# Kernel optimization log

Measured on AMD Instinct MI355X. Metric: run time of the kernel, lower is better.

The kernel has to match this reference:

```python
import jax, jax.numpy as jnp
import numpy as np

N = 8192
W_MEAN, W_VAR = 0.15, 0.25
DELTA_THETA_S = 30.0
B_S = 0.5
R_I = 18.0
F_V = 0.12
DELTA_V = 12.0
THETA_INIT = 30.0
E_L0, C_M0, G0, TAU_G0 = -65.0, 1.0, 0.7, 2.0


def setup_inputs() -> dict:
    key = jax.random.key(0)
    k_x, k_v, k_g, k_w = jax.random.split(key, 4)
    x_in = jax.random.normal(k_x, (N,), dtype=jnp.float32)
    v = jax.random.normal(k_v, (N,), dtype=jnp.float32)
    g = jax.random.uniform(k_g, (N,), dtype=jnp.float32)
    theta_s = THETA_INIT * jnp.ones((N,), dtype=jnp.float32)
    w = W_MEAN - W_VAR + 2.0 * W_VAR * jax.random.uniform(k_w, (N, N), dtype=jnp.float32)
    E_L = E_L0 * jnp.ones((N,), dtype=jnp.float32)
    C_m = C_M0 * jnp.ones((N,), dtype=jnp.float32)
    G = G0 * jnp.ones((N,), dtype=jnp.float32)
    tau_g = TAU_G0 * jnp.ones((N,), dtype=jnp.float32)
    return {"x_in": x_in, "v": v, "g": g, "theta_s": theta_s, "w": w,
            "E_L": E_L, "C_m": C_m, "G": G, "tau_g": tau_g}


def reference(x_in, v, g, theta_s, w, E_L, C_m, G, tau_g):
    # One LIF_R step.  I: [N] = w @ g + x_in
    I = w @ g + x_in
    dv = (G * (E_L - v) + I * R_I) / C_m
    v_next = v + dv
    spiked_soft = jax.nn.sigmoid(v_next - theta_s)           # differentiable spike surrogate
    spiked = (v_next >= theta_s).astype(v.dtype)             # hard spike indicator
    not_spiked = 1.0 - spiked
    v_reset = E_L + F_V * (v - E_L) - DELTA_V
    v_new = spiked * v_reset + not_spiked * v_next
    theta_new = spiked * (theta_s + DELTA_THETA_S) + not_spiked * ((1.0 - B_S) * theta_s)
    g_new = g - not_spiked * g / tau_g
    # original returns (self.v, self.spiked); g/theta updated as hidden state
    del theta_new, g_new
    return (v_new, spiked_soft)
```

## Files before the change

kernel.cpp:

```cpp
#include <hip/hip_runtime.h>
#include <math.h>

#define NN 8192
#define ROWS_PER_BLOCK 4

typedef float f32x4 __attribute__((ext_vector_type(4)));

__global__ __launch_bounds__(256, 4)
void lif_r_kernel(const float* __restrict__ x_in,
                  const float* __restrict__ v,
                  const float* __restrict__ g,
                  const float* __restrict__ theta_s,
                  const float* __restrict__ w,
                  const float* __restrict__ E_L,
                  const float* __restrict__ C_m,
                  const float* __restrict__ Gc,
                  const float* __restrict__ tau_g,
                  float* __restrict__ out)
{
    const int wave = threadIdx.x >> 6;
    const int lane = threadIdx.x & 63;
    const int row  = blockIdx.x * ROWS_PER_BLOCK + wave;

    const f32x4* __restrict__ wrow =
        reinterpret_cast<const f32x4*>(w + (size_t)row * NN);
    const f32x4* __restrict__ g4 = reinterpret_cast<const f32x4*>(g);

    float acc = 0.0f;
    for (int t = 0; t < 4; ++t) {
#pragma unroll
        for (int u = 0; u < 8; ++u) {
            const int idx = lane + 64 * (t * 8 + u);
            const f32x4 wv = __builtin_nontemporal_load(&wrow[idx]);
            const f32x4 gv = g4[idx];
            acc += wv.x * gv.x + wv.y * gv.y + wv.z * gv.z + wv.w * gv.w;
        }
    }

#pragma unroll
    for (int off = 32; off > 0; off >>= 1)
        acc += __shfl_down(acc, off, 64);

    if (lane == 0) {
        const float I      = acc + x_in[row];
        const float vv     = v[row];
        const float el     = E_L[row];
        const float th     = theta_s[row];
        const float dv     = (Gc[row] * (el - vv) + I * 18.0f) / C_m[row];
        const float v_next = vv + dv;
        const float d      = v_next - th;
        const float spk_soft = 1.0f / (1.0f + expf(-d));
        const float spiked   = (v_next >= th) ? 1.0f : 0.0f;
        const float v_reset  = el + 0.12f * (vv - el) - 12.0f;
        const float v_new    = spiked * v_reset + (1.0f - spiked) * v_next;
        out[row]      = v_new;
        out[NN + row] = spk_soft;
        (void)tau_g;
    }
}

extern "C" void kernel_launch(void* const* d_in, const int* in_sizes, int n_in,
                              void* d_out, int out_size, void* d_ws, size_t ws_size,
                              hipStream_t stream)
{
    const float* x_in    = (const float*)d_in[0];
    const float* v       = (const float*)d_in[1];
    const float* g       = (const float*)d_in[2];
    const float* theta_s = (const float*)d_in[3];
    const float* w       = (const float*)d_in[4];
    const float* E_L     = (const float*)d_in[5];
    const float* C_m     = (const float*)d_in[6];
    const float* Gc      = (const float*)d_in[7];
    const float* tau_g   = (const float*)d_in[8];
    float* out = (float*)d_out;

    dim3 grid(NN / ROWS_PER_BLOCK);
    dim3 block(256);
    lif_r_kernel<<<grid, block, 0, stream>>>(x_in, v, g, theta_s, w,
                                             E_L, C_m, Gc, tau_g, out);
}
```

Baseline: 46.04 us.

## Process four rows per wave to reuse g vector loads in GEMV

Each wave now computes four output rows at once, loading each g chunk once and reusing it for four w rows. The aim is to cut redundant g loads and raise memory-level parallelism per wave. The grid shrinks fourfold, occupancy hints drop from 4 to 2, and the nontemporal loads on w are replaced by ordinary loads, which may pollute cache for the 256MB streaming matrix.

```diff
diff --git a/kernel.cpp b/kernel.cpp
--- a/kernel.cpp
+++ b/kernel.cpp
@@ -2,11 +2,12 @@
 #include <math.h>
 
 #define NN 8192
-#define ROWS_PER_BLOCK 4
+#define ROWS_PER_WAVE 4
+#define WAVES_PER_BLOCK 4
 
 typedef float f32x4 __attribute__((ext_vector_type(4)));
 
-__global__ __launch_bounds__(256, 4)
+__global__ __launch_bounds__(256, 2)
 void lif_r_kernel(const float* __restrict__ x_in,
                   const float* __restrict__ v,
                   const float* __restrict__ g,
@@ -20,41 +21,59 @@
 {
     const int wave = threadIdx.x >> 6;
     const int lane = threadIdx.x & 63;
-    const int row  = blockIdx.x * ROWS_PER_BLOCK + wave;
+    const int row0 = (blockIdx.x * WAVES_PER_BLOCK + wave) * ROWS_PER_WAVE;
 
-    const f32x4* __restrict__ wrow =
-        reinterpret_cast<const f32x4*>(w + (size_t)row * NN);
     const f32x4* __restrict__ g4 = reinterpret_cast<const f32x4*>(g);
+    const f32x4* __restrict__ wr0 = reinterpret_cast<const f32x4*>(w + (size_t)(row0 + 0) * NN);
+    const f32x4* __restrict__ wr1 = reinterpret_cast<const f32x4*>(w + (size_t)(row0 + 1) * NN);
+    const f32x4* __restrict__ wr2 = reinterpret_cast<const f32x4*>(w + (size_t)(row0 + 2) * NN);
+    const f32x4* __restrict__ wr3 = reinterpret_cast<const f32x4*>(w + (size_t)(row0 + 3) * NN);
 
-    float acc = 0.0f;
-    for (int t = 0; t < 4; ++t) {
+    float acc0 = 0.0f, acc1 = 0.0f, acc2 = 0.0f, acc3 = 0.0f;
+
+    for (int t = 0; t < 8; ++t) {
 #pragma unroll
-        for (int u = 0; u < 8; ++u) {
-            const int idx = lane + 64 * (t * 8 + u);
-            const f32x4 wv = __builtin_nontemporal_load(&wrow[idx]);
+        for (int u = 0; u < 4; ++u) {
+            const int idx = lane + 64 * (t * 4 + u);
             const f32x4 gv = g4[idx];
-            acc += wv.x * gv.x + wv.y * gv.y + wv.z * gv.z + wv.w * gv.w;
+            const f32x4 a = wr0[idx];
+            const f32x4 b = wr1[idx];
+            const f32x4 c = wr2[idx];
+            const f32x4 d = wr3[idx];
+            acc0 += a.x * gv.x + a.y * gv.y + a.z * gv.z + a.w * gv.w;
+            acc1 += b.x * gv.x + b.y * gv.y + b.z * gv.z + b.w * gv.w;
+            acc2 += c.x * gv.x + c.y * gv.y + c.z * gv.z + c.w * gv.w;
+            acc3 += d.x * gv.x + d.y * gv.y + d.z * gv.z + d.w * gv.w;
         }
     }
 
 #pragma unroll
-    for (int off = 32; off > 0; off >>= 1)
-        acc += __shfl_down(acc, off, 64);
+    for (int off = 32; off > 0; off >>= 1) {
+        acc0 += __shfl_down(acc0, off, 64);
+        acc1 += __shfl_down(acc1, off, 64);
+        acc2 += __shfl_down(acc2, off, 64);
+        acc3 += __shfl_down(acc3, off, 64);
+    }
 
     if (lane == 0) {
-        const float I      = acc + x_in[row];
-        const float vv     = v[row];
-        const float el     = E_L[row];
-        const float th     = theta_s[row];
-        const float dv     = (Gc[row] * (el - vv) + I * 18.0f) / C_m[row];
-        const float v_next = vv + dv;
-        const float d      = v_next - th;
-        const float spk_soft = 1.0f / (1.0f + expf(-d));
-        const float spiked   = (v_next >= th) ? 1.0f : 0.0f;
-        const float v_reset  = el + 0.12f * (vv - el) - 12.0f;
-        const float v_new    = spiked * v_reset + (1.0f - spiked) * v_next;
-        out[row]      = v_new;
-        out[NN + row] = spk_soft;
+        const float accs[4] = {acc0, acc1, acc2, acc3};
+#pragma unroll
+        for (int r = 0; r < 4; ++r) {
+            const int row = row0 + r;
+            const float I      = accs[r] + x_in[row];
+            const float vv     = v[row];
+            const float el     = E_L[row];
+            const float th     = theta_s[row];
+            const float dv     = (Gc[row] * (el - vv) + I * 18.0f) / C_m[row];
+            const float v_next = vv + dv;
+            const float dlt    = v_next - th;
+            const float spk_soft = 1.0f / (1.0f + expf(-dlt));
+            const float spiked   = (v_next >= th) ? 1.0f : 0.0f;
+            const float v_reset  = el + 0.12f * (vv - el) - 12.0f;
+            const float v_new    = spiked * v_reset + (1.0f - spiked) * v_next;
+            out[row]      = v_new;
+            out[NN + row] = spk_soft;
+        }
         (void)tau_g;
     }
 }
@@ -74,7 +93,7 @@
     const float* tau_g   = (const float*)d_in[8];
     float* out = (float*)d_out;
 
-    dim3 grid(NN / ROWS_PER_BLOCK);
+    dim3 grid(NN / (ROWS_PER_WAVE * WAVES_PER_BLOCK));
     dim3 block(256);
     lif_r_kernel<<<grid, block, 0, stream>>>(x_in, v, g, theta_s, w,
                                              E_L, C_m, Gc, tau_g, out);
```

After: 53.33 us. 1.16x slower.
